# Kernel tuning notes

Measured on AMD Instinct MI355X. Metric: run time of the kernel, lower is better.

The kernel has to match this reference:

```python
import jax, jax.numpy as jnp
import numpy as np

N, E, F, C, K, N_G, N_M = 100000, 600000, 6, 128, 3, 2, 2


def setup_inputs() -> dict:
    key = jax.random.key(0)
    ks = jax.random.split(key, 12)
    x = jax.random.normal(ks[0], (N, F), dtype=jnp.float32)
    edge_index = jax.random.randint(ks[1], (2, E), 0, N, dtype=jnp.int32)
    s = 0.05
    W0 = jax.random.normal(ks[2], (F, C), dtype=jnp.float32) * s
    b0 = jnp.zeros((C,), dtype=jnp.float32)
    # TAGConv: per layer, K+1 hop weights (no per-lin bias) + one shared bias
    W_tag = jax.random.normal(ks[3], (N_G, K + 1, C, C), dtype=jnp.float32) * s
    b_tag = jnp.zeros((N_G, C), dtype=jnp.float32)
    W_mlp = jax.random.normal(ks[4], (N_M, C, C), dtype=jnp.float32) * s
    b_mlp = jnp.zeros((N_M, C), dtype=jnp.float32)
    W1 = jax.random.normal(ks[5], (C, 1), dtype=jnp.float32) * s
    b1 = jnp.zeros((1,), dtype=jnp.float32)
    return {"x": x, "edge_index": edge_index, "W0": W0, "b0": b0,
            "W_tag": W_tag, "b_tag": b_tag, "W_mlp": W_mlp, "b_mlp": b_mlp,
            "W1": W1, "b1": b1}


def reference(x, edge_index, W0, b0, W_tag, b_tag, W_mlp, b_mlp, W1, b1):
    row, col = edge_index[0], edge_index[1]  # source -> target
    n = x.shape[0]
    # GCN-style symmetric normalization, no self-loops (PyG TAGConv default)
    deg = jax.ops.segment_sum(jnp.ones((row.shape[0],), x.dtype), col, num_segments=n)
    dis = jnp.where(deg > 0, jax.lax.rsqrt(jnp.maximum(deg, 1.0)), 0.0)
    norm = dis[row] * dis[col]  # [E]

    h = jax.nn.relu(x @ W0 + b0)  # lin0

    for g in range(W_tag.shape[0]):  # n_G TAGConv layers
        out = h @ W_tag[g, 0]
        xk = h
        for k in range(1, W_tag.shape[1]):  # K hops
            msg = norm[:, None] * xk[row]           # [E, C] gather
            xk = jax.ops.segment_sum(msg, col, num_segments=n)  # scatter-add
            out = out + xk @ W_tag[g, k]
        h = jax.nn.relu(out + b_tag[g])

    for m in range(W_mlp.shape[0]):  # mlp block
        h = jax.nn.relu(h @ W_mlp[m] + b_mlp[m])

    return jax.nn.relu(h @ W1 + b1)  # [N, 1]
```

## Files before the change

kernel.cpp:

```cpp
#include <hip/hip_runtime.h>

#define NN 100000
#define NP 100096
#define NE 600000
#define CC 128

typedef __attribute__((ext_vector_type(4))) float f32x4;
typedef _Float16 h8 __attribute__((ext_vector_type(8)));
typedef _Float16 h2 __attribute__((ext_vector_type(2)));


__global__ void k_deg(const int* __restrict__ col, int* __restrict__ deg) {
  int e = blockIdx.x * 256 + threadIdx.x;
  if (e < NE) atomicAdd(&deg[col[e]], 1);
}

__global__ void k_dis(const int* __restrict__ deg, float* __restrict__ dis) {
  int n = blockIdx.x * 256 + threadIdx.x;
  if (n >= NP) return;
  int d = (n < NN) ? deg[n] : 0;
  dis[n] = (d > 0) ? rsqrtf((float)d) : 0.0f;
}

__global__ void k_scan1(const int* __restrict__ deg, int* __restrict__ rowptr,
                        int* __restrict__ bsum) {
  __shared__ int s[1024];
  int t = threadIdx.x;
  int i = blockIdx.x * 1024 + t;
  int v = (i < NN) ? deg[i] : 0;
  s[t] = v;
  __syncthreads();
  #pragma unroll
  for (int off = 1; off < 1024; off <<= 1) {
    int tv = (t >= off) ? s[t - off] : 0;
    __syncthreads();
    s[t] += tv;
    __syncthreads();
  }
  if (i < NN) rowptr[i] = s[t] - v;
  if (t == 1023) bsum[blockIdx.x] = s[1023];
}

__global__ void k_scan2(const int* __restrict__ bsum, int* __restrict__ bsum2) {
  __shared__ int s[128];
  int t = threadIdx.x;
  int v = (t < 98) ? bsum[t] : 0;
  s[t] = v;
  __syncthreads();
  #pragma unroll
  for (int off = 1; off < 128; off <<= 1) {
    int tv = (t >= off) ? s[t - off] : 0;
    __syncthreads();
    s[t] += tv;
    __syncthreads();
  }
  bsum2[t] = s[t] - v;
}

__global__ void k_scan3(int* __restrict__ rowptr, const int* __restrict__ bsum2) {
  int i = blockIdx.x * 1024 + threadIdx.x;
  if (i < NN) rowptr[i] += bsum2[blockIdx.x];
}

__global__ void k_rptail(int* __restrict__ rowptr) {
  int i = NN + blockIdx.x * 256 + threadIdx.x;
  if (i < NP + 8) rowptr[i] = NE;
}

__global__ void k_fill(const int* __restrict__ row, const int* __restrict__ col,
                       const float* __restrict__ dis, const int* __restrict__ rowptr,
                       int* __restrict__ cnt, int2* __restrict__ csr) {
  int e = blockIdx.x * 256 + threadIdx.x;
  if (e >= NE) return;
  int c = col[e], r = row[e];
  int pos = rowptr[c] + atomicAdd(&cnt[c], 1);
  int2 v;
  v.x = r * CC;
  v.y = __float_as_int(dis[r] * dis[c]);
  csr[pos] = v;
}


__global__ void k_lin0(const float* __restrict__ x, const float* __restrict__ W0,
                       const float* __restrict__ b0, _Float16* __restrict__ h) {
  int idx = blockIdx.x * 256 + threadIdx.x;
  int n = idx >> 7, c = idx & 127;
  if (n >= NP) return;
  float v = 0.0f;
  if (n < NN) {
    v = b0[c];
    #pragma unroll
    for (int f = 0; f < 6; ++f) v = fmaf(x[n * 6 + f], W0[f * CC + c], v);
    v = fmaxf(v, 0.0f);
  }
  h[idx] = (_Float16)v;
}


__global__ void k_wconv(const float* __restrict__ src, _Float16* __restrict__ dst, int K) {
  int tid = blockIdx.x * 256 + threadIdx.x;
  if (tid >= K * 128) return;
  int e = tid & 7, l = (tid >> 3) & 63, nb = (tid >> 9) & 7, kb = tid >> 12;
  int k = kb * 32 + (l >> 4) * 8 + e;
  int c = nb * 16 + (l & 15);
  dst[tid] = (_Float16)src[k * 128 + c];
}


__global__ __launch_bounds__(256) void k_prop(const int* __restrict__ rowptr,
                                              const int2* __restrict__ csr,
                                              const _Float16* __restrict__ xin,
                                              _Float16* __restrict__ xout) {
  int gid = blockIdx.x * 256 + threadIdx.x;
  int wv = gid >> 6;
  int lane = gid & 63;
  int n0 = wv * 4;
  if (n0 >= NP) return;
  int b0 = rowptr[n0], b1 = rowptr[n0 + 1], b2 = rowptr[n0 + 2],
      b3 = rowptr[n0 + 3], b4 = rowptr[n0 + 4];
  int e4 = b4 - b0;

  int2 ew; ew.x = 0; ew.y = 0;
  int gl = 0;
  if (lane < e4) {
    int pos = b0 + lane;
    ew = csr[pos];
    gl = (pos >= b1) + (pos >= b2) + (pos >= b3);
  }

  float a00 = 0, a01 = 0, a10 = 0, a11 = 0, a20 = 0, a21 = 0, a30 = 0, a31 = 0;
  int nb = e4 < 64 ? e4 : 64;
  for (int j = 0; j < nb; j += 8) {
    #pragma unroll
    for (int u = 0; u < 8; ++u) {
      int off = __shfl(ew.x, j + u);
      float w = __uint_as_float(__shfl(ew.y, j + u));
      int gg = __shfl(gl, j + u);
      h2 v = *reinterpret_cast<const h2*>(&xin[off + lane * 2]);
      float v0 = (float)v[0], v1 = (float)v[1];
      float w0 = (gg == 0) ? w : 0.0f;
      float w1 = (gg == 1) ? w : 0.0f;
      float w2 = (gg == 2) ? w : 0.0f;
      float w3 = (gg == 3) ? w : 0.0f;
      a00 += w0 * v0; a01 += w0 * v1;
      a10 += w1 * v0; a11 += w1 * v1;
      a20 += w2 * v0; a21 += w2 * v1;
      a30 += w3 * v0; a31 += w3 * v1;
    }
  }
  for (int j = 64; j < e4; ++j) {
    int pos = b0 + j;
    int2 e2 = csr[pos];
    float w = __uint_as_float(e2.y);
    int gg = (pos >= b1) + (pos >= b2) + (pos >= b3);
    h2 v = *reinterpret_cast<const h2*>(&xin[e2.x + lane * 2]);
    float v0 = (float)v[0], v1 = (float)v[1];
    float w0 = (gg == 0) ? w : 0.0f;
    float w1 = (gg == 1) ? w : 0.0f;
    float w2 = (gg == 2) ? w : 0.0f;
    float w3 = (gg == 3) ? w : 0.0f;
    a00 += w0 * v0; a01 += w0 * v1;
    a10 += w1 * v0; a11 += w1 * v1;
    a20 += w2 * v0; a21 += w2 * v1;
    a30 += w3 * v0; a31 += w3 * v1;
  }

  h2 o;
  o[0] = (_Float16)a00; o[1] = (_Float16)a01;
  *reinterpret_cast<h2*>(&xout[(size_t)(n0 + 0) * CC + lane * 2]) = o;
  o[0] = (_Float16)a10; o[1] = (_Float16)a11;
  *reinterpret_cast<h2*>(&xout[(size_t)(n0 + 1) * CC + lane * 2]) = o;
  o[0] = (_Float16)a20; o[1] = (_Float16)a21;
  *reinterpret_cast<h2*>(&xout[(size_t)(n0 + 2) * CC + lane * 2]) = o;
  o[0] = (_Float16)a30; o[1] = (_Float16)a31;
  *reinterpret_cast<h2*>(&xout[(size_t)(n0 + 3) * CC + lane * 2]) = o;
}


template<int KB, bool BR>
__global__ __launch_bounds__(256) void k_mm(const _Float16* __restrict__ X0,
                                            const _Float16* __restrict__ X1,
                                            const _Float16* __restrict__ X2,
                                            const _Float16* __restrict__ X3,
                                            const _Float16* __restrict__ Wp,
                                            const float* __restrict__ bias,
                                            _Float16* __restrict__ Y) {
  __shared__ _Float16 lds[128 * 128];
  int t = threadIdx.x;
  int w = t >> 6, l = t & 63;
  int lr = l & 15, lk = l >> 4;
  int m0w = (w & 1) * 64;
  int nb0 = (w >> 1) * 4;
  long row0 = (long)blockIdx.x * 128;
  const _Float16* Xs[4] = {X0, X1, X2, X3};

  f32x4 acc[4][4];
  #pragma unroll
  for (int m = 0; m < 4; ++m)
    #pragma unroll
    for (int n = 0; n < 4; ++n) acc[m][n] = (f32x4){0.f, 0.f, 0.f, 0.f};

  #pragma unroll
  for (int xi = 0; xi < KB; ++xi) {
    const _Float16* __restrict__ xb = Xs[xi];
    #pragma unroll
    for (int i = 0; i < 8; ++i) {
      int li = i * 256 + t;
      int r = li >> 4, ck = li & 15;
      int cs = ck ^ (r & 7);
      const _Float16* src = xb + (size_t)(row0 + r) * CC + cs * 8;
      _Float16* dst = lds + ((size_t)i * 2048 + (size_t)(t & 192) * 8);
      __builtin_amdgcn_global_load_lds((const __attribute__((address_space(1))) void*)src,
                                       (__attribute__((address_space(3))) void*)dst,
                                       16, 0, 0);
    }
    __syncthreads();

    #pragma unroll
    for (int kk = 0; kk < 4; ++kk) {
      int kb = xi * 4 + kk;
      h8 a[4], b[4];
      #pragma unroll
      for (int m = 0; m < 4; ++m) {
        int R = m0w + m * 16 + lr;
        a[m] = *reinterpret_cast<const h8*>(&lds[R * 128 + (((kk * 4 + lk) ^ (lr & 7)) << 3)]);
      }
      #pragma unroll
      for (int n = 0; n < 4; ++n)
        b[n] = *reinterpret_cast<const h8*>(&Wp[((size_t)(kb * 8 + nb0 + n) * 64 + l) * 8]);
      #pragma unroll
      for (int m = 0; m < 4; ++m)
        #pragma unroll
        for (int n = 0; n < 4; ++n)
          acc[m][n] = __builtin_amdgcn_mfma_f32_16x16x32_f16(a[m], b[n], acc[m][n], 0, 0, 0);
    }
    __syncthreads();
  }

  int r0 = m0w + lk * 4;
  long rb = row0 + r0;
  #pragma unroll
  for (int m = 0; m < 4; ++m) {
    #pragma unroll
    for (int n = 0; n < 4; ++n) {
      int c = (nb0 + n) * 16 + lr;
      float bv = BR ? bias[c] : 0.0f;
      #pragma unroll
      for (int q = 0; q < 4; ++q) {
        float v = acc[m][n][q] + bv;
        if (BR) v = fmaxf(v, 0.0f);
        Y[(rb + m * 16 + q) * CC + c] = (_Float16)v;
      }
    }
  }
}


__global__ void k_head(const _Float16* __restrict__ h, const float* __restrict__ W1,
                       const float* __restrict__ b1, float* __restrict__ out) {
  int gid = blockIdx.x * 256 + threadIdx.x;
  int wid = gid >> 6, lane = gid & 63;
  if (wid >= NN) return;
  const _Float16* hp = &h[wid * CC];
  float v = (float)hp[lane] * W1[lane] + (float)hp[lane + 64] * W1[lane + 64];
  #pragma unroll
  for (int o = 32; o > 0; o >>= 1) v += __shfl_down(v, o);
  if (lane == 0) out[wid] = fmaxf(v + b1[0], 0.0f);
}


extern "C" void kernel_launch(void* const* d_in, const int* in_sizes, int n_in,
                              void* d_out, int out_size, void* d_ws, size_t ws_size,
                              hipStream_t stream) {
  const float* x     = (const float*)d_in[0];
  const int*   ei    = (const int*)d_in[1];
  const float* W0    = (const float*)d_in[2];
  const float* b0    = (const float*)d_in[3];
  const float* W_tag = (const float*)d_in[4];
  const float* b_tag = (const float*)d_in[5];
  const float* W_mlp = (const float*)d_in[6];
  const float* b_mlp = (const float*)d_in[7];
  const float* W1    = (const float*)d_in[8];
  const float* b1    = (const float*)d_in[9];
  const int* row = ei;
  const int* col = ei + NE;

  char* p = (char*)d_ws;
  auto carve = [&](size_t bytes) { void* r = (void*)p; p += (bytes + 255) & ~(size_t)255; return r; };
  _Float16* hA   = (_Float16*)carve((size_t)NP * CC * 2);
  _Float16* hB   = (_Float16*)carve((size_t)NP * CC * 2);
  _Float16* x1   = (_Float16*)carve((size_t)NP * CC * 2);
  _Float16* x2   = (_Float16*)carve((size_t)NP * CC * 2);
  _Float16* x3   = (_Float16*)carve((size_t)NP * CC * 2);
  _Float16* WpT0 = (_Float16*)carve((size_t)512 * CC * 2);
  _Float16* WpT1 = (_Float16*)carve((size_t)512 * CC * 2);
  _Float16* WpM0 = (_Float16*)carve((size_t)CC * CC * 2);
  _Float16* WpM1 = (_Float16*)carve((size_t)CC * CC * 2);
  float* dis     = (float*)carve((size_t)NP * 4);
  int*   deg     = (int*)carve((size_t)NP * 4);
  int*   rowptr  = (int*)carve((size_t)(NP + 8) * 4);
  int*   cnt     = (int*)carve((size_t)NN * 4);
  int*   bsum    = (int*)carve(512);
  int*   bsum2   = (int*)carve(512);
  int2*  csr     = (int2*)carve((size_t)NE * 8);

  hipMemsetAsync(deg, 0, (size_t)NP * 4, stream);
  hipMemsetAsync(cnt, 0, (size_t)NN * 4, stream);

  k_deg<<<(NE + 255) / 256, 256, 0, stream>>>(col, deg);
  k_dis<<<(NP + 255) / 256, 256, 0, stream>>>(deg, dis);
  k_scan1<<<98, 1024, 0, stream>>>(deg, rowptr, bsum);
  k_scan2<<<1, 128, 0, stream>>>(bsum, bsum2);
  k_scan3<<<98, 1024, 0, stream>>>(rowptr, bsum2);
  k_rptail<<<1, 256, 0, stream>>>(rowptr);
  k_fill<<<(NE + 255) / 256, 256, 0, stream>>>(row, col, dis, rowptr, cnt, csr);

  k_wconv<<<(512 * CC + 255) / 256, 256, 0, stream>>>(W_tag,            WpT0, 512);
  k_wconv<<<(512 * CC + 255) / 256, 256, 0, stream>>>(W_tag + 512 * CC, WpT1, 512);
  k_wconv<<<(CC * CC + 255) / 256, 256, 0, stream>>>(W_mlp,             WpM0, 128);
  k_wconv<<<(CC * CC + 255) / 256, 256, 0, stream>>>(W_mlp + CC * CC,   WpM1, 128);

  k_lin0<<<NP * CC / 256, 256, 0, stream>>>(x, W0, b0, hA);

  const int GB = NP / 128;
  const int PB = (NP / 4) * 64 / 256;

  _Float16* hc = hA;
  _Float16* hn = hB;
  const _Float16* WpT[2] = {WpT0, WpT1};
  for (int g = 0; g < 2; ++g) {
    k_prop<<<PB, 256, 0, stream>>>(rowptr, csr, hc, x1);
    k_prop<<<PB, 256, 0, stream>>>(rowptr, csr, x1, x2);
    k_prop<<<PB, 256, 0, stream>>>(rowptr, csr, x2, x3);
    k_mm<4, true><<<GB, 256, 0, stream>>>(hc, x1, x2, x3, WpT[g], b_tag + (size_t)g * CC, hn);
    _Float16* tmp = hc; hc = hn; hn = tmp;
  }

  k_mm<1, true><<<GB, 256, 0, stream>>>(hc, nullptr, nullptr, nullptr, WpM0, b_mlp, hn);
  { _Float16* tmp = hc; hc = hn; hn = tmp; }
  k_mm<1, true><<<GB, 256, 0, stream>>>(hc, nullptr, nullptr, nullptr, WpM1, b_mlp + CC, hn);
  { _Float16* tmp = hc; hc = hn; hn = tmp; }

  k_head<<<(NN * 64) / 256, 256, 0, stream>>>(hc, W1, b1, (float*)d_out);
}
```

Measured before the change: 402.1 us.

## Fuse MLP layers and head into one kernel, double-buffer TAGConv GEMM staging

Two MLP GEMMs and the output head now run in one kernel. The intermediate activations stay in LDS, which avoids two full N×128 fp16 round trips through global memory and two launches. The TAGConv GEMM double-buffers its LDS staging so the next hop's tile loads overlap the MFMAs on the current one, at the cost of twice the LDS per block. Small launches are also merged: the rowptr-tail kernel folds into scan2, the memsets combine, and the weight conversions batch into two launches.

```diff
diff --git a/kernel.cpp b/kernel.cpp
--- a/kernel.cpp
+++ b/kernel.cpp
@@ -41,9 +41,11 @@
   if (t == 1023) bsum[blockIdx.x] = s[1023];
 }
 
-__global__ void k_scan2(const int* __restrict__ bsum, int* __restrict__ bsum2) {
+__global__ void k_scan2(const int* __restrict__ bsum, int* __restrict__ bsum2,
+                        int* __restrict__ rowptr) {
+  int t = threadIdx.x;
+  if (t < NP + 8 - NN) rowptr[NN + t] = NE;
   __shared__ int s[128];
-  int t = threadIdx.x;
   int v = (t < 98) ? bsum[t] : 0;
   s[t] = v;
   __syncthreads();
@@ -60,11 +62,6 @@
 __global__ void k_scan3(int* __restrict__ rowptr, const int* __restrict__ bsum2) {
   int i = blockIdx.x * 1024 + threadIdx.x;
   if (i < NN) rowptr[i] += bsum2[blockIdx.x];
-}
-
-__global__ void k_rptail(int* __restrict__ rowptr) {
-  int i = NN + blockIdx.x * 256 + threadIdx.x;
-  if (i < NP + 8) rowptr[i] = NE;
 }
 
 __global__ void k_fill(const int* __restrict__ row, const int* __restrict__ col,
@@ -185,6 +182,94 @@
                                             const _Float16* __restrict__ Wp,
                                             const float* __restrict__ bias,
                                             _Float16* __restrict__ Y) {
+  __shared__ _Float16 lds[2][128 * 128];
+  int t = threadIdx.x;
+  int w = t >> 6, l = t & 63;
+  int lr = l & 15, lk = l >> 4;
+  int m0w = (w & 1) * 64;
+  int nb0 = (w >> 1) * 4;
+  long row0 = (long)blockIdx.x * 128;
+  const _Float16* Xs[4] = {X0, X1, X2, X3};
+
+  auto stage = [&](int buf, const _Float16* __restrict__ xb) {
+    #pragma unroll
+    for (int i = 0; i < 8; ++i) {
+      int li = i * 256 + t;
+      int r = li >> 4, ck = li & 15;
+      int cs = ck ^ (r & 7);
+      const _Float16* src = xb + (size_t)(row0 + r) * CC + cs * 8;
+      _Float16* dst = &lds[buf][i * 2048 + (t & 192) * 8];
+      __builtin_amdgcn_global_load_lds((const __attribute__((address_space(1))) void*)src,
+                                       (__attribute__((address_space(3))) void*)dst,
+                                       16, 0, 0);
+    }
+  };
+
+  f32x4 acc[4][4];
+  #pragma unroll
+  for (int m = 0; m < 4; ++m)
+    #pragma unroll
+    for (int n = 0; n < 4; ++n) acc[m][n] = (f32x4){0.f, 0.f, 0.f, 0.f};
+
+  stage(0, Xs[0]);
+  #pragma unroll
+  for (int xi = 0; xi < KB; ++xi) {
+    if (xi + 1 < KB) {
+      stage((xi + 1) & 1, Xs[xi + 1]);
+      asm volatile("s_waitcnt vmcnt(8)" ::: "memory");
+    } else {
+      asm volatile("s_waitcnt vmcnt(0)" ::: "memory");
+    }
+    __builtin_amdgcn_sched_barrier(0);
+    __builtin_amdgcn_s_barrier();
+    const _Float16* __restrict__ lb = lds[xi & 1];
+
+    #pragma unroll
+    for (int kk = 0; kk < 4; ++kk) {
+      int kb = xi * 4 + kk;
+      h8 a[4], b[4];
+      #pragma unroll
+      for (int m = 0; m < 4; ++m) {
+        int R = m0w + m * 16 + lr;
+        a[m] = *reinterpret_cast<const h8*>(&lb[R * 128 + (((kk * 4 + lk) ^ (lr & 7)) << 3)]);
+      }
+      #pragma unroll
+      for (int n = 0; n < 4; ++n)
+        b[n] = *reinterpret_cast<const h8*>(&Wp[((size_t)(kb * 8 + nb0 + n) * 64 + l) * 8]);
+      #pragma unroll
+      for (int m = 0; m < 4; ++m)
+        #pragma unroll
+        for (int n = 0; n < 4; ++n)
+          acc[m][n] = __builtin_amdgcn_mfma_f32_16x16x32_f16(a[m], b[n], acc[m][n], 0, 0, 0);
+    }
+    __builtin_amdgcn_s_barrier();
+  }
+
+  int r0 = m0w + lk * 4;
+  long rb = row0 + r0;
+  #pragma unroll
+  for (int m = 0; m < 4; ++m) {
+    #pragma unroll
+    for (int n = 0; n < 4; ++n) {
+      int c = (nb0 + n) * 16 + lr;
+      float bv = BR ? bias[c] : 0.0f;
+      #pragma unroll
+      for (int q = 0; q < 4; ++q) {
+        float v = acc[m][n][q] + bv;
+        if (BR) v = fmaxf(v, 0.0f);
+        Y[(rb + m * 16 + q) * CC + c] = (_Float16)v;
+      }
+    }
+  }
+}
+
+
+__global__ __launch_bounds__(256) void k_tail(const _Float16* __restrict__ X,
+                                              const _Float16* __restrict__ WpM,
+                                              const float* __restrict__ b_mlp,
+                                              const float* __restrict__ W1,
+                                              const float* __restrict__ b1,
+                                              float* __restrict__ out) {
   __shared__ _Float16 lds[128 * 128];
   int t = threadIdx.x;
   int w = t >> 6, l = t & 63;
@@ -192,33 +277,29 @@
   int m0w = (w & 1) * 64;
   int nb0 = (w >> 1) * 4;
   long row0 = (long)blockIdx.x * 128;
-  const _Float16* Xs[4] = {X0, X1, X2, X3};
+
+  #pragma unroll
+  for (int i = 0; i < 8; ++i) {
+    int li = i * 256 + t;
+    int r = li >> 4, ck = li & 15;
+    int cs = ck ^ (r & 7);
+    const _Float16* src = X + (size_t)(row0 + r) * CC + cs * 8;
+    _Float16* dst = &lds[i * 2048 + (t & 192) * 8];
+    __builtin_amdgcn_global_load_lds((const __attribute__((address_space(1))) void*)src,
+                                     (__attribute__((address_space(3))) void*)dst,
+                                     16, 0, 0);
+  }
+  __syncthreads();
 
   f32x4 acc[4][4];
   #pragma unroll
-  for (int m = 0; m < 4; ++m)
-    #pragma unroll
-    for (int n = 0; n < 4; ++n) acc[m][n] = (f32x4){0.f, 0.f, 0.f, 0.f};
-
-  #pragma unroll
-  for (int xi = 0; xi < KB; ++xi) {
-    const _Float16* __restrict__ xb = Xs[xi];
-    #pragma unroll
-    for (int i = 0; i < 8; ++i) {
-      int li = i * 256 + t;
-      int r = li >> 4, ck = li & 15;
-      int cs = ck ^ (r & 7);
-      const _Float16* src = xb + (size_t)(row0 + r) * CC + cs * 8;
-      _Float16* dst = lds + ((size_t)i * 2048 + (size_t)(t & 192) * 8);
-      __builtin_amdgcn_global_load_lds((const __attribute__((address_space(1))) void*)src,
-                                       (__attribute__((address_space(3))) void*)dst,
-                                       16, 0, 0);
-    }
-    __syncthreads();
-
+  for (int ph = 0; ph < 2; ++ph) {
+    #pragma unroll
+    for (int m = 0; m < 4; ++m)
+      #pragma unroll
+      for (int n = 0; n < 4; ++n) acc[m][n] = (f32x4){0.f, 0.f, 0.f, 0.f};
     #pragma unroll
     for (int kk = 0; kk < 4; ++kk) {
-      int kb = xi * 4 + kk;
       h8 a[4], b[4];
       #pragma unroll
       for (int m = 0; m < 4; ++m) {
@@ -227,7 +308,7 @@
       }
       #pragma unroll
       for (int n = 0; n < 4; ++n)
-        b[n] = *reinterpret_cast<const h8*>(&Wp[((size_t)(kb * 8 + nb0 + n) * 64 + l) * 8]);
+        b[n] = *reinterpret_cast<const h8*>(&WpM[((size_t)((ph * 4 + kk) * 8 + nb0 + n) * 64 + l) * 8]);
       #pragma unroll
       for (int m = 0; m < 4; ++m)
         #pragma unroll
@@ -235,37 +316,37 @@
           acc[m][n] = __builtin_amdgcn_mfma_f32_16x16x32_f16(a[m], b[n], acc[m][n], 0, 0, 0);
     }
     __syncthreads();
-  }
-
-  int r0 = m0w + lk * 4;
-  long rb = row0 + r0;
-  #pragma unroll
-  for (int m = 0; m < 4; ++m) {
-    #pragma unroll
-    for (int n = 0; n < 4; ++n) {
-      int c = (nb0 + n) * 16 + lr;
-      float bv = BR ? bias[c] : 0.0f;
-      #pragma unroll
-      for (int q = 0; q < 4; ++q) {
-        float v = acc[m][n][q] + bv;
-        if (BR) v = fmaxf(v, 0.0f);
-        Y[(rb + m * 16 + q) * CC + c] = (_Float16)v;
+    #pragma unroll
+    for (int m = 0; m < 4; ++m) {
+      #pragma unroll
+      for (int n = 0; n < 4; ++n) {
+        int c = (nb0 + n) * 16 + lr;
+        float bv = b_mlp[ph * 128 + c];
+        #pragma unroll
+        for (int q = 0; q < 4; ++q) {
+          int R = m0w + m * 16 + lk * 4 + q;
+          float v = fmaxf(acc[m][n][q] + bv, 0.0f);
+          int gc = c >> 3;
+          lds[R * 128 + ((gc ^ (R & 7)) << 3) + (c & 7)] = (_Float16)v;
+        }
       }
     }
-  }
-}
-
-
-__global__ void k_head(const _Float16* __restrict__ h, const float* __restrict__ W1,
-                       const float* __restrict__ b1, float* __restrict__ out) {
-  int gid = blockIdx.x * 256 + threadIdx.x;
-  int wid = gid >> 6, lane = gid & 63;
-  if (wid >= NN) return;
-  const _Float16* hp = &h[wid * CC];
-  float v = (float)hp[lane] * W1[lane] + (float)hp[lane + 64] * W1[lane + 64];
-  #pragma unroll
-  for (int o = 32; o > 0; o >>= 1) v += __shfl_down(v, o);
-  if (lane == 0) out[wid] = fmaxf(v + b1[0], 0.0f);
+    __syncthreads();
+  }
+
+  int c0 = 2 * l;
+  float w1a = W1[c0], w1b = W1[c0 + 1];
+  float b1v = b1[0];
+  int gH = c0 >> 3, eo = c0 & 7;
+  for (int rr = 0; rr < 32; ++rr) {
+    int R = w * 32 + rr;
+    long grow = row0 + R;
+    h2 v = *reinterpret_cast<const h2*>(&lds[R * 128 + ((gH ^ (R & 7)) << 3) + eo]);
+    float s = (float)v[0] * w1a + (float)v[1] * w1b;
+    #pragma unroll
+    for (int o = 32; o > 0; o >>= 1) s += __shfl_down(s, o);
+    if (l == 0 && grow < NN) out[grow] = fmaxf(s + b1v, 0.0f);
+  }
 }
 
 
@@ -292,33 +373,28 @@
   _Float16* x1   = (_Float16*)carve((size_t)NP * CC * 2);
   _Float16* x2   = (_Float16*)carve((size_t)NP * CC * 2);
   _Float16* x3   = (_Float16*)carve((size_t)NP * CC * 2);
-  _Float16* WpT0 = (_Float16*)carve((size_t)512 * CC * 2);
-  _Float16* WpT1 = (_Float16*)carve((size_t)512 * CC * 2);
-  _Float16* WpM0 = (_Float16*)carve((size_t)CC * CC * 2);
-  _Float16* WpM1 = (_Float16*)carve((size_t)CC * CC * 2);
+  _Float16* WpT  = (_Float16*)carve((size_t)1024 * CC * 2);
+  _Float16* WpM  = (_Float16*)carve((size_t)256 * CC * 2);
   float* dis     = (float*)carve((size_t)NP * 4);
-  int*   deg     = (int*)carve((size_t)NP * 4);
+  int*   dc      = (int*)carve((size_t)(NP + NN) * 4);
+  int*   deg     = dc;
+  int*   cnt     = dc + NP;
   int*   rowptr  = (int*)carve((size_t)(NP + 8) * 4);
-  int*   cnt     = (int*)carve((size_t)NN * 4);
   int*   bsum    = (int*)carve(512);
   int*   bsum2   = (int*)carve(512);
   int2*  csr     = (int2*)carve((size_t)NE * 8);
 
-  hipMemsetAsync(deg, 0, (size_t)NP * 4, stream);
-  hipMemsetAsync(cnt, 0, (size_t)NN * 4, stream);
+  hipMemsetAsync(dc, 0, (size_t)(NP + NN) * 4, stream);
 
   k_deg<<<(NE + 255) / 256, 256, 0, stream>>>(col, deg);
   k_dis<<<(NP + 255) / 256, 256, 0, stream>>>(deg, dis);
   k_scan1<<<98, 1024, 0, stream>>>(deg, rowptr, bsum);
-  k_scan2<<<1, 128, 0, stream>>>(bsum, bsum2);
+  k_scan2<<<1, 128, 0, stream>>>(bsum, bsum2, rowptr);
   k_scan3<<<98, 1024, 0, stream>>>(rowptr, bsum2);
-  k_rptail<<<1, 256, 0, stream>>>(rowptr);
   k_fill<<<(NE + 255) / 256, 256, 0, stream>>>(row, col, dis, rowptr, cnt, csr);
 
-  k_wconv<<<(512 * CC + 255) / 256, 256, 0, stream>>>(W_tag,            WpT0, 512);
-  k_wconv<<<(512 * CC + 255) / 256, 256, 0, stream>>>(W_tag + 512 * CC, WpT1, 512);
-  k_wconv<<<(CC * CC + 255) / 256, 256, 0, stream>>>(W_mlp,             WpM0, 128);
-  k_wconv<<<(CC * CC + 255) / 256, 256, 0, stream>>>(W_mlp + CC * CC,   WpM1, 128);
+  k_wconv<<<(1024 * CC + 255) / 256, 256, 0, stream>>>(W_tag, WpT, 1024);
+  k_wconv<<<(256 * CC + 255) / 256, 256, 0, stream>>>(W_mlp, WpM, 256);
 
   k_lin0<<<NP * CC / 256, 256, 0, stream>>>(x, W0, b0, hA);
 
@@ -327,19 +403,14 @@
 
   _Float16* hc = hA;
   _Float16* hn = hB;
-  const _Float16* WpT[2] = {WpT0, WpT1};
   for (int g = 0; g < 2; ++g) {
     k_prop<<<PB, 256, 0, stream>>>(rowptr, csr, hc, x1);
     k_prop<<<PB, 256, 0, stream>>>(rowptr, csr, x1, x2);
     k_prop<<<PB, 256, 0, stream>>>(rowptr, csr, x2, x3);
-    k_mm<4, true><<<GB, 256, 0, stream>>>(hc, x1, x2, x3, WpT[g], b_tag + (size_t)g * CC, hn);
+    k_mm<4, true><<<GB, 256, 0, stream>>>(hc, x1, x2, x3, WpT + (size_t)g * 512 * CC,
+                                          b_tag + (size_t)g * CC, hn);
     _Float16* tmp = hc; hc = hn; hn = tmp;
   }
 
-  k_mm<1, true><<<GB, 256, 0, stream>>>(hc, nullptr, nullptr, nullptr, WpM0, b_mlp, hn);
-  { _Float16* tmp = hc; hc = hn; hn = tmp; }
-  k_mm<1, true><<<GB, 256, 0, stream>>>(hc, nullptr, nullptr, nullptr, WpM1, b_mlp + CC, hn);
-  { _Float16* tmp = hc; hc = hn; hn = tmp; }
-
-  k_head<<<(NN * 64) / 256, 256, 0, stream>>>(hc, W1, b1, (float*)d_out);
-}
+  k_tail<<<GB, 256, 0, stream>>>(hc, WpM, b_mlp, W1, b1, (float*)d_out);
+}
```

New measurement: 379.3 us. 1.06x faster.
